# Optimization experiments

Hardware: AMD Instinct MI355X
Metric: run time of the kernel (lower is better)

## Reference

```python
import jax, jax.numpy as jnp
import numpy as np

B, L, D_MODEL = 2, 4096, 1024
D_INNER = 2048  # expand * d_model
D_CONV = 4


def setup_inputs() -> dict:
    key = jax.random.key(0)
    ks = jax.random.split(key, 7)
    return {
        "hidden_states": jax.random.normal(ks[0], (B, L, D_MODEL), jnp.float32),
        "W_in": jax.random.normal(ks[1], (2 * D_INNER, D_MODEL), jnp.float32) * 0.02,
        "conv_w": jax.random.normal(ks[2], (D_INNER, D_CONV), jnp.float32) * 0.1,
        "conv_b": jax.random.normal(ks[3], (D_INNER,), jnp.float32) * 0.1,
        "k_ssm": jax.random.normal(ks[4], (D_INNER, L), jnp.float32) * 0.02,  # materialized SSM kernel (channels=1)
        "D_skip": jax.random.normal(ks[5], (D_INNER,), jnp.float32),
        "W_out": jax.random.normal(ks[6], (D_MODEL, D_INNER), jnp.float32) * 0.02,
    }


def _silu(x):
    return x * jax.nn.sigmoid(x)


def reference(hidden_states, W_in, conv_w, conv_b, k_ssm, D_skip, W_out):
    Bq, Lq, _ = hidden_states.shape
    # in_proj (no bias): (B, L, d_model) -> (B, 2*d_inner, L)
    xz = jnp.einsum('bld,ed->bel', hidden_states, W_in)
    x, z = jnp.split(xz, 2, axis=1)  # each (B, d_inner, L)

    # causal depthwise conv1d (pad left d_conv-1) + SiLU (causal_conv1d_fn)
    xp = jnp.pad(x, ((0, 0), (0, 0), (D_CONV - 1, 0)))
    xc = conv_b[None, :, None]
    for j in range(D_CONV):
        xc = xc + conv_w[None, :, j, None] * xp[:, :, j:j + Lq]
    x = _silu(xc)

    # FFT long convolution (l_kernel = L, n = 2L), channels = 1
    n = 2 * Lq
    x_f = jnp.fft.rfft(x, n=n)            # (B, H, n//2+1) complex
    k_f = jnp.fft.rfft(k_ssm, n=n)        # (H, n//2+1)
    y = jnp.fft.irfft(x_f * k_f[None], n=n)[..., :Lq]  # (B, H, L)

    # D skip connection
    y = y + x * D_skip[None, :, None]

    # gating with SiLU(z)
    y = y * _silu(z)

    # out_proj (no bias): (B, H, L) -> (B, L, d_model)
    return jnp.einsum('bhl,dh->bld', y, W_out)
```

## Files before the change

### kernel.cpp

```cpp
#include <hip/hip_runtime.h>
#include <hip/hip_bf16.h>
#include <math.h>

#define B_SZ 2
#define L_SZ 4096
#define DM   1024
#define DI   2048
#define E_SZ 4096
#define DC   4

typedef unsigned short u16;
typedef __attribute__((ext_vector_type(8))) short short8;
typedef __attribute__((ext_vector_type(4))) float f32x4;

__device__ __forceinline__ float silu_f(float v) {
    return v / (1.0f + __expf(-v));
}

__device__ __forceinline__ void split_bf16(float x, u16& h, u16& l) {
    unsigned u  = __float_as_uint(x);
    unsigned hb = u & 0xFFFF0000u;
    h = (u16)(hb >> 16);
    float lf = x - __uint_as_float(hb);
    l = (u16)(__float_as_uint(lf) >> 16);
}
__device__ __forceinline__ float bf2f(u16 h) {
    return __uint_as_float(((unsigned)h) << 16);
}

__device__ __forceinline__ void gld_lds16(const u16* g, u16* l) {
    __builtin_amdgcn_global_load_lds(
        (const __attribute__((address_space(1))) unsigned int*)g,
        (__attribute__((address_space(3))) unsigned int*)l, 16, 0, 0);
}

__global__ __launch_bounds__(256) void pack_rm(
    const float* __restrict__ X, u16* __restrict__ H, u16* __restrict__ Lo,
    int ldx, int r16n, long sX, long sOut)
{
    const long cid = (long)blockIdx.x * 256 + threadIdx.x;
    const int  qc  = (int)(cid & 63);
    const long blk = cid >> 6;
    const int  r16 = (int)(blk % r16n);
    const int  k32 = (int)(blk / r16n);
    const int  q = qc >> 4, m = qc & 15;

    const float* src = X + blockIdx.y * sX + (long)(r16 * 16 + m) * ldx + k32 * 32 + q * 8;
    float4 v0 = *(const float4*)src;
    float4 v1 = *(const float4*)(src + 4);
    float v[8] = {v0.x,v0.y,v0.z,v0.w,v1.x,v1.y,v1.z,v1.w};

    u16 hs[8], ls[8];
    #pragma unroll
    for (int j = 0; j < 8; ++j) split_bf16(v[j], hs[j], ls[j]);

    const long o = blockIdx.y * sOut + cid * 8;
    *(uint4*)&H[o]  = *(const uint4*)hs;
    *(uint4*)&Lo[o] = *(const uint4*)ls;
}

__global__ __launch_bounds__(256) void gemm_mfma(
    const u16* __restrict__ Ah, const u16* __restrict__ Al,
    const u16* __restrict__ Bh, const u16* __restrict__ Bl,
    float* __restrict__ C,
    int r16A, int r16B, long sA, long sB, long sC,
    int ldc, int nk32)
{
    __shared__ alignas(16) u16 sm[4][4096];

    const int tid  = threadIdx.x;
    const int wv   = tid >> 6, lane = tid & 63;
    const long zb  = blockIdx.z;

    const u16* srcs0 = Ah + zb * sA;
    const u16* srcs1 = Al + zb * sA;
    const u16* srcs2 = Bh + zb * sB;
    const u16* srcs3 = Bl + zb * sB;
    const u16* mysrc = (wv == 0) ? srcs0 : (wv == 1) ? srcs1 : (wv == 2) ? srcs2 : srcs3;
    const int  rblk  = (wv < 2) ? blockIdx.x * 8 : blockIdx.y * 8;
    const int  r16c  = (wv < 2) ? r16A : r16B;
    u16* myl = sm[wv];

    const int wr = wv >> 1, wc = wv & 1;

    f32x4 acc[4][4];
    #pragma unroll
    for (int i = 0; i < 4; ++i)
        #pragma unroll
        for (int j = 0; j < 4; ++j)
            #pragma unroll
            for (int r = 0; r < 4; ++r) acc[i][j][r] = 0.f;

    for (int s = 0; s < nk32; ++s) {
        if (s) __syncthreads();
        {
            const u16* g = mysrc + (((long)s * r16c + rblk) << 9) + lane * 8;
            #pragma unroll
            for (int i = 0; i < 8; ++i)
                gld_lds16(g + (i << 9), myl + (i << 9));
        }
        __syncthreads();

        short8 afh[4], afl[4], bfh[4], bfl[4];
        const int aoff = (wr * 4) * 512 + lane * 8;
        const int boff = (wc * 4) * 512 + lane * 8;
        #pragma unroll
        for (int t = 0; t < 4; ++t) {
            afh[t] = *(const short8*)&sm[0][aoff + t * 512];
            afl[t] = *(const short8*)&sm[1][aoff + t * 512];
            bfh[t] = *(const short8*)&sm[2][boff + t * 512];
            bfl[t] = *(const short8*)&sm[3][boff + t * 512];
        }
        #pragma unroll
        for (int i = 0; i < 4; ++i)
            #pragma unroll
            for (int j = 0; j < 4; ++j) {
                acc[i][j] = __builtin_amdgcn_mfma_f32_16x16x32_bf16(afh[i], bfh[j], acc[i][j], 0, 0, 0);
                acc[i][j] = __builtin_amdgcn_mfma_f32_16x16x32_bf16(afh[i], bfl[j], acc[i][j], 0, 0, 0);
                acc[i][j] = __builtin_amdgcn_mfma_f32_16x16x32_bf16(afl[i], bfh[j], acc[i][j], 0, 0, 0);
            }
    }

    const int m_ = lane & 15, q_ = lane >> 4;
    float* Cb = C + zb * sC;
    const int row00 = blockIdx.x * 128 + wr * 64 + q_ * 4;
    const int col0  = blockIdx.y * 128 + wc * 64 + m_;
    #pragma unroll
    for (int i = 0; i < 4; ++i)
        #pragma unroll
        for (int j = 0; j < 4; ++j) {
            const long base = (long)(row00 + i * 16) * ldc + col0 + j * 16;
            #pragma unroll
            for (int r = 0; r < 4; ++r)
                Cb[base + (long)r * ldc] = acc[i][j][r];
        }
}

__global__ __launch_bounds__(256) void conv_silu_split(
    const float* __restrict__ xz, const float* __restrict__ conv_w,
    const float* __restrict__ conv_b,
    u16* __restrict__ xh_gl, u16* __restrict__ xl_gl)
{
    const long gid = (long)blockIdx.x * 256 + threadIdx.x;
    const int  q   = (int)(gid % (L_SZ / 4));
    const long bc  = gid / (L_SZ / 4);
    const int  ch  = (int)(bc % DI);
    const int  b   = (int)(bc / DI);

    const float* row = xz + ((long)b * E_SZ + ch) * L_SZ;
    const int l0 = q * 4;

    float4 cur  = *(const float4*)&row[l0];
    float4 prev = q ? *(const float4*)&row[l0 - 4] : make_float4(0.f, 0.f, 0.f, 0.f);

    const float w0 = conv_w[ch*DC+0], w1 = conv_w[ch*DC+1];
    const float w2 = conv_w[ch*DC+2], w3 = conv_w[ch*DC+3];
    const float bias = conv_b[ch];

    float o[4];
    o[0] = silu_f(bias + w0*prev.y + w1*prev.z + w2*prev.w + w3*cur.x);
    o[1] = silu_f(bias + w0*prev.z + w1*prev.w + w2*cur.x  + w3*cur.y);
    o[2] = silu_f(bias + w0*prev.w + w1*cur.x  + w2*cur.y  + w3*cur.z);
    o[3] = silu_f(bias + w0*cur.x  + w1*cur.y  + w2*cur.z  + w3*cur.w);

    unsigned long long hp = 0ull, lp = 0ull;
    #pragma unroll
    for (int r = 0; r < 4; ++r) {
        u16 h, l; split_bf16(o[r], h, l);
        hp |= ((unsigned long long)h) << (16*r);
        lp |= ((unsigned long long)l) << (16*r);
    }
    const long base = ((long)b * DI + ch) * L_SZ + l0;
    *(unsigned long long*)&xh_gl[base] = hp;
    *(unsigned long long*)&xl_gl[base] = lp;
}

__global__ __launch_bounds__(128, 2) void longconv_mfma(
    u16* __restrict__ xh_gl, u16* __restrict__ xl_gl,
    const float* __restrict__ xz,  const float* __restrict__ k_ssm,
    const float* __restrict__ D_skip)
{
    __shared__ u16 Xh[2][4352];
    __shared__ u16 Xl[2][4352];

    const int lane = threadIdx.x & 63;
    const int wv   = threadIdx.x >> 6;
    const int wc   = blockIdx.x * 2 + wv;
    const int ch   = wc & (DI - 1);
    const int b    = wc >> 11;

    u16*         xhr  = xh_gl + ((long)b * DI + ch) * L_SZ;
    u16*         xlr  = xl_gl + ((long)b * DI + ch) * L_SZ;
    const float* krow = k_ssm + (long)ch * L_SZ;

    u16* XH = Xh[wv];
    u16* XL = Xl[wv];

    if (lane < 32) {
        uint4 z = make_uint4(0u, 0u, 0u, 0u);
        *(uint4*)&XH[lane * 8] = z;
        *(uint4*)&XL[lane * 8] = z;
    }
    #pragma unroll
    for (int it = 0; it < 8; ++it) {
        const int idx = it * 64 + lane;
        *(uint4*)&XH[256 + idx * 8] = ((const uint4*)xhr)[idx];
        *(uint4*)&XL[256 + idx * 8] = ((const uint4*)xlr)[idx];
    }
    __syncthreads();

    const int m_ = lane & 15;
    const int q_ = lane >> 4;
    const int dq = m_ - 8 * q_ + ((q_ >= 2) ? 32 : 0);
    const int xoff_lane = 256 + 16 * m_ + 8 * q_ - ((q_ >= 2) ? 32 : 0);

    f32x4 acc[16];
    #pragma unroll
    for (int t = 0; t < 16; ++t)
        #pragma unroll
        for (int r = 0; r < 4; ++r) acc[t][r] = 0.f;

    float kn[8];
    #pragma unroll
    for (int e = 0; e < 8; ++e) {
        const int ki = dq - e;
        kn[e] = (ki >= 0) ? krow[ki] : 0.0f;
    }

    for (int c = 0; c < 128; ++c) {
        float kv[8];
        #pragma unroll
        for (int e = 0; e < 8; ++e) kv[e] = kn[e];
        if (c < 127) {
            #pragma unroll
            for (int e = 0; e < 8; ++e) {
                const int ki = 32 * (c + 1) + dq - e;
                kn[e] = (ki >= 0) ? krow[ki] : 0.0f;
            }
        }

        short8 ah, al;
        #pragma unroll
        for (int e = 0; e < 8; ++e) {
            u16 h, l; split_bf16(kv[e], h, l);
            ah[e] = (short)h; al[e] = (short)l;
        }

        const int xbase = xoff_lane - 32 * c;
        #pragma unroll
        for (int t = 0; t < 16; ++t) {
            if (8 * t >= c - 7) {
                short8 bh = *(const short8*)&XH[xbase + 256 * t];
                short8 bl = *(const short8*)&XL[xbase + 256 * t];
                acc[t] = __builtin_amdgcn_mfma_f32_16x16x32_bf16(ah, bh, acc[t], 0, 0, 0);
                acc[t] = __builtin_amdgcn_mfma_f32_16x16x32_bf16(ah, bl, acc[t], 0, 0, 0);
                acc[t] = __builtin_amdgcn_mfma_f32_16x16x32_bf16(al, bh, acc[t], 0, 0, 0);
            }
        }
    }

    const float  Ds   = D_skip[ch];
    const float* zrow = xz + ((long)b * E_SZ + DI + ch) * L_SZ;

    #pragma unroll
    for (int t = 0; t < 16; ++t) {
        const int l0 = 256 * t + 16 * m_ + 4 * q_;
        float4 zv = *(const float4*)&zrow[l0];
        float zt[4] = { zv.x, zv.y, zv.z, zv.w };
        unsigned long long hp = 0ull, lp = 0ull;
        #pragma unroll
        for (int r = 0; r < 4; ++r) {
            const float xf = bf2f(XH[256 + l0 + r]) + bf2f(XL[256 + l0 + r]);
            const float o  = (acc[t][r] + Ds * xf) * silu_f(zt[r]);
            u16 h, l; split_bf16(o, h, l);
            hp |= ((unsigned long long)h) << (16*r);
            lp |= ((unsigned long long)l) << (16*r);
        }
        *(unsigned long long*)&xhr[l0] = hp;
        *(unsigned long long*)&xlr[l0] = lp;
    }
}

__global__ __launch_bounds__(256) void pack_y(
    const u16* __restrict__ Yh, const u16* __restrict__ Yl,
    u16* __restrict__ OH, u16* __restrict__ OL, long sOut)
{
    __shared__ u16 T[2][32][136];
    const int t  = threadIdx.x;
    const int l0 = blockIdx.x * 128;
    const int h0 = blockIdx.y * 32;
    const int b  = blockIdx.z;

    const u16* yb_h = Yh + ((long)b * DI + h0) * L_SZ + l0;
    const u16* yb_l = Yl + ((long)b * DI + h0) * L_SZ + l0;

    #pragma unroll
    for (int i = 0; i < 2; ++i) {
        const int c = t + 256 * i;
        const int row = c >> 4, col = (c & 15) * 8;
        *(uint4*)&T[0][row][col] = *(const uint4*)&yb_h[(long)row * L_SZ + col];
        *(uint4*)&T[1][row][col] = *(const uint4*)&yb_l[(long)row * L_SZ + col];
    }
    __syncthreads();

    u16* outs[2] = { OH + b * sOut, OL + b * sOut };
    #pragma unroll
    for (int p = 0; p < 2; ++p) {
        #pragma unroll
        for (int i = 0; i < 2; ++i) {
            const int c = t + 256 * i;
            const int r16b = c >> 6, qc = c & 63;
            const int q = qc >> 4, m = qc & 15;
            const int l = r16b * 16 + m;
            u16 vals[8];
            #pragma unroll
            for (int j = 0; j < 8; ++j) vals[j] = T[p][q * 8 + j][l];
            const long o = ((long)(blockIdx.y * 256 + blockIdx.x * 8 + r16b) << 9) + qc * 8;
            *(uint4*)&outs[p][o] = *(const uint4*)vals;
        }
    }
}

extern "C" void kernel_launch(void* const* d_in, const int* in_sizes, int n_in,
                              void* d_out, int out_size, void* d_ws, size_t ws_size,
                              hipStream_t stream)
{
    const float* hidden = (const float*)d_in[0];
    const float* W_in   = (const float*)d_in[1];
    const float* conv_w = (const float*)d_in[2];
    const float* conv_b = (const float*)d_in[3];
    const float* k_ssm  = (const float*)d_in[4];
    const float* D_skip = (const float*)d_in[5];
    const float* W_out  = (const float*)d_in[6];
    float* out = (float*)d_out;

    char* ws = (char*)d_ws;
    float* xz  = (float*)ws;
    u16*   xh  = (u16*)(ws + 134217728);
    u16*   xl  = (u16*)(ws + 167772160);
    u16*   WinH  = (u16*)(ws + 201326592);
    u16*   WinL  = WinH + 4194304;
    u16*   WoutH = (u16*)(ws + 201326592);
    u16*   WoutL = WoutH + 2097152;
    u16*   hidH  = (u16*)(ws + 218103808);
    u16*   hidL  = hidH + 8388608;
    u16*   yAh   = (u16*)ws;
    u16*   yAl   = yAh + 8388608;

    pack_rm<<<dim3(2048, 1), 256, 0, stream>>>(W_in, WinH, WinL, DM, 256, 0L, 0L);
    pack_rm<<<dim3(2048, B_SZ), 256, 0, stream>>>(hidden, hidH, hidL, DM, 256,
        (long)L_SZ * DM, 4194304L);

    gemm_mfma<<<dim3(32, 32, B_SZ), 256, 0, stream>>>(
        WinH, WinL, hidH, hidL, xz,
        256, 256, 0L, 4194304L, (long)E_SZ * L_SZ, L_SZ, 32);

    conv_silu_split<<<dim3((unsigned)((long)B_SZ*DI*(L_SZ/4)/256)), 256, 0, stream>>>(
        xz, conv_w, conv_b, xh, xl);

    longconv_mfma<<<dim3((B_SZ * DI) / 2), 128, 0, stream>>>(
        xh, xl, xz, k_ssm, D_skip);

    pack_rm<<<dim3(1024, 1), 256, 0, stream>>>(W_out, WoutH, WoutL, DI, 64, 0L, 0L);

    pack_y<<<dim3(32, 64, B_SZ), 256, 0, stream>>>(
        xh, xl, yAh, yAl, 33554432L);

    gemm_mfma<<<dim3(32, 8, B_SZ), 256, 0, stream>>>(
        yAh, yAl, WoutH, WoutL, out,
        256, 64, 33554432L, 0L, (long)L_SZ * DM, DM, 64);
}
```

Before: 675.4 us.

## Pre-split SSM kernel to bf16 pairs and use one-wave blocks with direct LDS loads

Adds a kernel that splits k_ssm into bf16 high/low halves once, so the long-convolution loop no longer re-splits kernel taps per batch. The long-conv kernel becomes single-wave blocks (one channel each) and fills its LDS buffers with global_load_lds instead of register round-trips. The trade-off is an extra launch and extra global traffic for the split kernel arrays, plus 2-byte scattered loads of the kernel taps in the inner loop. The pre-split buffers reuse the workspace region of the hidden-state packs, which are dead by the time they are written.

```diff
diff --git a/kernel.cpp b/kernel.cpp
--- a/kernel.cpp
+++ b/kernel.cpp
@@ -32,6 +32,23 @@
     __builtin_amdgcn_global_load_lds(
         (const __attribute__((address_space(1))) unsigned int*)g,
         (__attribute__((address_space(3))) unsigned int*)l, 16, 0, 0);
+}
+
+__global__ __launch_bounds__(256) void ksplit(
+    const float* __restrict__ k_ssm, u16* __restrict__ kh, u16* __restrict__ kl)
+{
+    const long i4 = ((long)blockIdx.x * 256 + threadIdx.x) * 4;
+    float4 v = *(const float4*)&k_ssm[i4];
+    float vv[4] = { v.x, v.y, v.z, v.w };
+    unsigned long long hp = 0ull, lp = 0ull;
+    #pragma unroll
+    for (int r = 0; r < 4; ++r) {
+        u16 h, l; split_bf16(vv[r], h, l);
+        hp |= ((unsigned long long)h) << (16*r);
+        lp |= ((unsigned long long)l) << (16*r);
+    }
+    *(unsigned long long*)&kh[i4] = hp;
+    *(unsigned long long*)&kl[i4] = lp;
 }
 
 __global__ __launch_bounds__(256) void pack_rm(
@@ -175,26 +192,24 @@
     *(unsigned long long*)&xl_gl[base] = lp;
 }
 
-__global__ __launch_bounds__(128, 2) void longconv_mfma(
+__global__ __launch_bounds__(64) void longconv_mfma(
     u16* __restrict__ xh_gl, u16* __restrict__ xl_gl,
-    const float* __restrict__ xz,  const float* __restrict__ k_ssm,
+    const float* __restrict__ xz,
+    const u16* __restrict__ kh_gl, const u16* __restrict__ kl_gl,
     const float* __restrict__ D_skip)
 {
-    __shared__ u16 Xh[2][4352];
-    __shared__ u16 Xl[2][4352];
-
-    const int lane = threadIdx.x & 63;
-    const int wv   = threadIdx.x >> 6;
-    const int wc   = blockIdx.x * 2 + wv;
+    __shared__ alignas(16) u16 XH[4352];
+    __shared__ alignas(16) u16 XL[4352];
+
+    const int lane = threadIdx.x;
+    const int wc   = blockIdx.x;
     const int ch   = wc & (DI - 1);
     const int b    = wc >> 11;
 
-    u16*         xhr  = xh_gl + ((long)b * DI + ch) * L_SZ;
-    u16*         xlr  = xl_gl + ((long)b * DI + ch) * L_SZ;
-    const float* krow = k_ssm + (long)ch * L_SZ;
-
-    u16* XH = Xh[wv];
-    u16* XL = Xl[wv];
+    u16*       xhr = xh_gl + ((long)b * DI + ch) * L_SZ;
+    u16*       xlr = xl_gl + ((long)b * DI + ch) * L_SZ;
+    const u16* khr = kh_gl + (long)ch * L_SZ;
+    const u16* klr = kl_gl + (long)ch * L_SZ;
 
     if (lane < 32) {
         uint4 z = make_uint4(0u, 0u, 0u, 0u);
@@ -203,10 +218,10 @@
     }
     #pragma unroll
     for (int it = 0; it < 8; ++it) {
-        const int idx = it * 64 + lane;
-        *(uint4*)&XH[256 + idx * 8] = ((const uint4*)xhr)[idx];
-        *(uint4*)&XL[256 + idx * 8] = ((const uint4*)xlr)[idx];
-    }
+        gld_lds16(xhr + it * 512 + lane * 8, &XH[256 + it * 512]);
+        gld_lds16(xlr + it * 512 + lane * 8, &XL[256 + it * 512]);
+    }
+    __builtin_amdgcn_s_waitcnt(0);
     __syncthreads();
 
     const int m_ = lane & 15;
@@ -220,30 +235,26 @@
         #pragma unroll
         for (int r = 0; r < 4; ++r) acc[t][r] = 0.f;
 
-    float kn[8];
+    u16 knh[8], knl[8];
     #pragma unroll
     for (int e = 0; e < 8; ++e) {
         const int ki = dq - e;
-        kn[e] = (ki >= 0) ? krow[ki] : 0.0f;
+        knh[e] = (ki >= 0) ? khr[ki] : (u16)0;
+        knl[e] = (ki >= 0) ? klr[ki] : (u16)0;
     }
 
     for (int c = 0; c < 128; ++c) {
-        float kv[8];
-        #pragma unroll
-        for (int e = 0; e < 8; ++e) kv[e] = kn[e];
+        short8 ah, al;
+        #pragma unroll
+        for (int e = 0; e < 8; ++e) { ah[e] = (short)knh[e]; al[e] = (short)knl[e]; }
+
         if (c < 127) {
+            const int kb = 32 * (c + 1) + dq;
             #pragma unroll
             for (int e = 0; e < 8; ++e) {
-                const int ki = 32 * (c + 1) + dq - e;
-                kn[e] = (ki >= 0) ? krow[ki] : 0.0f;
+                knh[e] = khr[kb - e];
+                knl[e] = klr[kb - e];
             }
-        }
-
-        short8 ah, al;
-        #pragma unroll
-        for (int e = 0; e < 8; ++e) {
-            u16 h, l; split_bf16(kv[e], h, l);
-            ah[e] = (short)h; al[e] = (short)l;
         }
 
         const int xbase = xoff_lane - 32 * c;
@@ -344,6 +355,8 @@
     u16*   WoutL = WoutH + 2097152;
     u16*   hidH  = (u16*)(ws + 218103808);
     u16*   hidL  = hidH + 8388608;
+    u16*   khp   = (u16*)(ws + 218103808);
+    u16*   klp   = khp + 8388608;
     u16*   yAh   = (u16*)ws;
     u16*   yAl   = yAh + 8388608;
 
@@ -355,11 +368,13 @@
         WinH, WinL, hidH, hidL, xz,
         256, 256, 0L, 4194304L, (long)E_SZ * L_SZ, L_SZ, 32);
 
+    ksplit<<<dim3((DI * L_SZ) / 1024), 256, 0, stream>>>(k_ssm, khp, klp);
+
     conv_silu_split<<<dim3((unsigned)((long)B_SZ*DI*(L_SZ/4)/256)), 256, 0, stream>>>(
         xz, conv_w, conv_b, xh, xl);
 
-    longconv_mfma<<<dim3((B_SZ * DI) / 2), 128, 0, stream>>>(
-        xh, xl, xz, k_ssm, D_skip);
+    longconv_mfma<<<dim3(B_SZ * DI), 64, 0, stream>>>(
+        xh, xl, xz, khp, klp, D_skip);
 
     pack_rm<<<dim3(1024, 1), 256, 0, stream>>>(W_out, WoutH, WoutL, DI, 64, 0L, 0L);
 
```

New measurement: 693.3 us. +2.6%, slower.
